# Performance work log

Measured on AMD Instinct MI355X. Metric: run time of the kernel, lower is better.

The kernel has to match this reference:

```python
import jax, jax.numpy as jnp
import numpy as np

N = 33_554_432  # 2^25 elements


def setup_inputs() -> dict:
    key = jax.random.key(0)
    k1, k2, k3 = jax.random.split(key, 3)
    a = jax.random.randint(k1, (N,), 0, 1_000_000, dtype=jnp.int32)
    b = jax.random.randint(k2, (N,), 0, 1_000_000, dtype=jnp.int32)
    p = jax.random.randint(k3, (N,), 1, 1_000_000, dtype=jnp.int32)  # p >= 1 (mod-by-zero undefined)
    W_gcd = jnp.ones((1,), dtype=jnp.float32)
    W_mod = jnp.ones((1,), dtype=jnp.float32)
    return {"a": a, "b": b, "p": p, "W_gcd": W_gcd, "W_mod": W_mod}


def _vectorized_gcd(a, b):
    """Elementwise Euclidean GCD on int32 arrays via lax.while_loop.

    Runs the classic (a, b) -> (b, a mod b) iteration in parallel over all
    lanes; finished lanes (b == 0) are held fixed with jnp.where. Converges
    in O(log(max_val)) iterations (<~45 for values below 2^31).
    """
    a = jnp.abs(a)
    b = jnp.abs(b)

    def cond(state):
        _, bb = state
        return jnp.any(bb != 0)

    def body(state):
        aa, bb = state
        safe_b = jnp.where(bb != 0, bb, 1)  # avoid div-by-zero on finished lanes
        new_a = jnp.where(bb != 0, bb, aa)
        new_b = jnp.where(bb != 0, aa % safe_b, 0)
        return (new_a, new_b)

    g, _ = jax.lax.while_loop(cond, body, (a, b))
    return g


def reference(a, b, p, W_gcd, W_mod):
    # gcd branch: elementwise GCD, cast to param dtype, scaled by W_gcd
    gcd_out = _vectorized_gcd(a, b).astype(W_gcd.dtype) * W_gcd  # [N]
    # mod branch: (a % p) * W_mod  (torch precedence: (a % p) * W_mod)
    mod_out = (a % p).astype(W_mod.dtype) * W_mod  # [N]
    return gcd_out, mod_out
```

## Files before the change

kernel.cpp:

```cpp
#include <hip/hip_runtime.h>


typedef int v4i __attribute__((ext_vector_type(4)));

__device__ __forceinline__ unsigned ffbl(unsigned x) {
    unsigned r;
    asm("v_ffbl_b32 %0, %1" : "=v"(r) : "v"(x));
    return r;
}

__device__ __forceinline__ v4i prefetch16(const v4i* p) {
    v4i r;
    asm volatile("global_load_dwordx4 %0, %1, off"
                 : "=v"(r) : "v"(p) : "memory");
    return r;
}

__global__ __launch_bounds__(256) void ntb_kernel(
    const v4i* __restrict__ a4, const v4i* __restrict__ b4,
    const v4i* __restrict__ p4,
    const float* __restrict__ Wg, const float* __restrict__ Wm,
    float4* __restrict__ gcd_out, float4* __restrict__ mod_out, int n4)
{
    const float wg = Wg[0];
    const float wm = Wm[0];
    const int stride = gridDim.x * blockDim.x;

    int i = blockIdx.x * blockDim.x + threadIdx.x;
    if (i >= n4) return;

    v4i av = a4[i];
    v4i bv = b4[i];
    v4i pv = p4[i];

    while (true) {
        const int inext = i + stride;
        const int idxn  = (inext < n4) ? inext : 0;
        const v4i av_n = prefetch16(a4 + idxn);
        const v4i bv_n = prefetch16(b4 + idxn);
        const v4i pv_n = prefetch16(p4 + idxn);

        {
            float mm[4];
            #pragma unroll
            for (int v = 0; v < 4; ++v) {
                const float af = (float)(unsigned)av[v];
                const float pf = (float)(unsigned)pv[v];
                const float q  = rintf(af * __builtin_amdgcn_rcpf(pf));
                float r = fmaf(-q, pf, af);
                r += (r < 0.0f) ? pf : 0.0f;
                mm[v] = r * wm;
            }
            float4 m; m.x = mm[0]; m.y = mm[1]; m.z = mm[2]; m.w = mm[3];
            mod_out[i] = m;
        }

        unsigned A[4], B[4], S[4];
        #pragma unroll
        for (int v = 0; v < 4; ++v) {
            A[v] = (unsigned)av[v];
            B[v] = (unsigned)bv[v];
            S[v] = ffbl(A[v] | B[v]);
            A[v] >>= (ffbl(A[v]) & 31u);
        }

        for (;;) {
            #pragma unroll
            for (int it = 0; it < 8; ++it) {
                #pragma unroll
                for (int v = 0; v < 4; ++v) {
                    const unsigned b  = B[v] >> (ffbl(B[v]) & 31u);
                    const unsigned nb = __usad(A[v], b, 0u);
                    A[v] = min(A[v], b);
                    B[v] = nb;
                }
            }
            if (!__any((A[0] | A[1] | A[2] | A[3]) != 0u)) break;
        }

        float4 g;
        g.x = (float)((A[0] | B[0]) << (S[0] & 31u)) * wg;
        g.y = (float)((A[1] | B[1]) << (S[1] & 31u)) * wg;
        g.z = (float)((A[2] | B[2]) << (S[2] & 31u)) * wg;
        g.w = (float)((A[3] | B[3]) << (S[3] & 31u)) * wg;
        gcd_out[i] = g;

        if (inext >= n4) break;

        asm volatile("s_waitcnt vmcnt(2)" ::: "memory");
        __builtin_amdgcn_sched_barrier(0);
        i = inext;
        av = av_n; bv = bv_n; pv = pv_n;
    }
}

extern "C" void kernel_launch(void* const* d_in, const int* in_sizes, int n_in,
                              void* d_out, int out_size, void* d_ws, size_t ws_size,
                              hipStream_t stream) {
    const int n  = in_sizes[0];
    const int n4 = n >> 2;

    const v4i* a4 = (const v4i*)d_in[0];
    const v4i* b4 = (const v4i*)d_in[1];
    const v4i* p4 = (const v4i*)d_in[2];
    const float* Wg = (const float*)d_in[3];
    const float* Wm = (const float*)d_in[4];

    float* out = (float*)d_out;
    float4* gcd_out = (float4*)out;
    float4* mod_out = (float4*)(out + n);

    const int block = 256;
    const int grid  = 4096;

    ntb_kernel<<<grid, block, 0, stream>>>(a4, b4, p4, Wg, Wm, gcd_out, mod_out, n4);
}
```

Measured before the change: 532.8 us.

## Drop manual prefetch, peel 32 unrolled GCD steps, double grid size

```diff
diff --git a/kernel.cpp b/kernel.cpp
--- a/kernel.cpp
+++ b/kernel.cpp
@@ -6,13 +6,6 @@
 __device__ __forceinline__ unsigned ffbl(unsigned x) {
     unsigned r;
     asm("v_ffbl_b32 %0, %1" : "=v"(r) : "v"(x));
-    return r;
-}
-
-__device__ __forceinline__ v4i prefetch16(const v4i* p) {
-    v4i r;
-    asm volatile("global_load_dwordx4 %0, %1, off"
-                 : "=v"(r) : "v"(p) : "memory");
     return r;
 }
 
@@ -26,19 +19,10 @@
     const float wm = Wm[0];
     const int stride = gridDim.x * blockDim.x;
 
-    int i = blockIdx.x * blockDim.x + threadIdx.x;
-    if (i >= n4) return;
-
-    v4i av = a4[i];
-    v4i bv = b4[i];
-    v4i pv = p4[i];
-
-    while (true) {
-        const int inext = i + stride;
-        const int idxn  = (inext < n4) ? inext : 0;
-        const v4i av_n = prefetch16(a4 + idxn);
-        const v4i bv_n = prefetch16(b4 + idxn);
-        const v4i pv_n = prefetch16(p4 + idxn);
+    for (int i = blockIdx.x * blockDim.x + threadIdx.x; i < n4; i += stride) {
+        const v4i av = a4[i];
+        const v4i bv = b4[i];
+        const v4i pv = p4[i];
 
         {
             float mm[4];
@@ -64,7 +48,18 @@
             A[v] >>= (ffbl(A[v]) & 31u);
         }
 
-        for (;;) {
+        #pragma unroll
+        for (int it = 0; it < 32; ++it) {
+            #pragma unroll
+            for (int v = 0; v < 4; ++v) {
+                const unsigned b  = B[v] >> (ffbl(B[v]) & 31u);
+                const unsigned nb = __usad(A[v], b, 0u);
+                A[v] = min(A[v], b);
+                B[v] = nb;
+            }
+        }
+
+        while (__any((A[0] | A[1] | A[2] | A[3]) != 0u)) {
             #pragma unroll
             for (int it = 0; it < 8; ++it) {
                 #pragma unroll
@@ -75,7 +70,6 @@
                     B[v] = nb;
                 }
             }
-            if (!__any((A[0] | A[1] | A[2] | A[3]) != 0u)) break;
         }
 
         float4 g;
@@ -84,13 +78,6 @@
         g.z = (float)((A[2] | B[2]) << (S[2] & 31u)) * wg;
         g.w = (float)((A[3] | B[3]) << (S[3] & 31u)) * wg;
         gcd_out[i] = g;
-
-        if (inext >= n4) break;
-
-        asm volatile("s_waitcnt vmcnt(2)" ::: "memory");
-        __builtin_amdgcn_sched_barrier(0);
-        i = inext;
-        av = av_n; bv = bv_n; pv = pv_n;
     }
 }
 
@@ -111,7 +98,7 @@
     float4* mod_out = (float4*)(out + n);
 
     const int block = 256;
-    const int grid  = 4096;
+    const int grid  = 8192;
 
     ntb_kernel<<<grid, block, 0, stream>>>(a4, b4, p4, Wg, Wm, gcd_out, mod_out, n4);
 }
```

Result: no change. 541.6 us (+1.6%).
